# Optimization experiments

Hardware: AMD Instinct MI355X
Metric: run time of the kernel (lower is better)

The kernel has to match this reference:

```python
import jax, jax.numpy as jnp
import numpy as np

DIM = 1024
N_HEADS = 16
HEAD_DIM = 64
SEQ = 2048
BATCH = 2


def setup_inputs() -> dict:
    key = jax.random.key(0)
    ks = jax.random.split(key, 7)
    scale = 1.0 / np.sqrt(DIM)
    return {
        "q": jax.random.normal(ks[0], (BATCH, SEQ, DIM), dtype=jnp.float32),
        "k": jax.random.normal(ks[1], (BATCH, SEQ, DIM), dtype=jnp.float32),
        "v": jax.random.normal(ks[2], (BATCH, SEQ, DIM), dtype=jnp.float32),
        "wq": jax.random.normal(ks[3], (DIM, DIM), dtype=jnp.float32) * scale,
        "wk": jax.random.normal(ks[4], (DIM, DIM), dtype=jnp.float32) * scale,
        "wv": jax.random.normal(ks[5], (DIM, DIM), dtype=jnp.float32) * scale,
        "wo": jax.random.normal(ks[6], (DIM, DIM), dtype=jnp.float32) * scale,
    }


def reference(q, k, v, wq, wk, wv, wo):
    B, S, D = q.shape
    # Linear layers: y = x @ W.T (torch nn.Linear convention)
    qh = (q @ wq.T).reshape(B, S, N_HEADS, HEAD_DIM).transpose(0, 2, 1, 3)  # [B,H,S,hd]
    kh = (k @ wk.T).reshape(B, S, N_HEADS, HEAD_DIM).transpose(0, 2, 1, 3)
    vh = (v @ wv.T).reshape(B, S, N_HEADS, HEAD_DIM).transpose(0, 2, 1, 3)
    score = jnp.einsum('bhqd,bhkd->bhqk', qh, kh) / jnp.sqrt(jnp.float32(HEAD_DIM))
    # causal mask: upper triangle (j > i) set to -inf
    causal = jnp.tril(jnp.ones((S, S), dtype=bool))
    score = jnp.where(causal[None, None], score, -jnp.inf)
    attn = jax.nn.softmax(score, axis=-1)
    out = jnp.einsum('bhqk,bhkd->bhqd', attn, vh)  # [B,H,S,hd]
    out = out.transpose(0, 2, 1, 3).reshape(B, S, D)
    return out @ wo.T
```

## Files before the change

kernel.cpp:

```cpp
#include <hip/hip_runtime.h>

typedef unsigned short u16;
typedef unsigned int   u32;
typedef __bf16 bf16x8 __attribute__((ext_vector_type(8)));
typedef float  f32x4  __attribute__((ext_vector_type(4)));
typedef unsigned short u16x4 __attribute__((ext_vector_type(4)));
typedef unsigned short u16x8 __attribute__((ext_vector_type(8)));
typedef unsigned int   u32x2 __attribute__((ext_vector_type(2)));
typedef unsigned int   u32x4 __attribute__((ext_vector_type(4)));

#define DIM   1024
#define SEQ   2048
#define NH    16
#define HD    64
#define NBATCH 2

#define NEG_INF (-__builtin_inff())


__device__ __forceinline__ u16 f2bf(float f) {
  unsigned u = __float_as_uint(f);
  unsigned r = (u + 0x7FFFu + ((u >> 16) & 1u)) >> 16;
  return (u16)r;
}

__device__ __forceinline__ void gload16(const void* g, void* lds_uniform) {
  __builtin_amdgcn_global_load_lds(
      (__attribute__((address_space(1))) void*)(size_t)g,
      (__attribute__((address_space(3))) void*)lds_uniform,
      16, 0, 0);
}


__global__ __launch_bounds__(256) void cvt_all(
    const float* __restrict__ q, const float* __restrict__ k, const float* __restrict__ v,
    const float* __restrict__ wq, const float* __restrict__ wk, const float* __restrict__ wv,
    const float* __restrict__ wo, u16* __restrict__ ws) {
  const size_t M = 1u << 20;
  int b = blockIdx.x;
  const float* src;
  u16* dst;
  int idx;
  if (b < 6144) {
    int t = b >> 11; idx = b & 2047;
    src = (t == 0) ? q : (t == 1) ? k : v;
    dst = ws + (size_t)t * 4 * M;
  } else {
    int t = (b - 6144) >> 9; idx = (b - 6144) & 511;
    src = (t == 0) ? wq : (t == 1) ? wk : (t == 2) ? wv : wo;
    dst = ws + (12 + (size_t)t) * M;
  }
  size_t i = ((size_t)idx * 256 + threadIdx.x) * 8;
  float4 a = *(const float4*)(src + i);
  float4 c = *(const float4*)(src + i + 4);
  u16x8 o;
  o[0] = f2bf(a.x); o[1] = f2bf(a.y); o[2] = f2bf(a.z); o[3] = f2bf(a.w);
  o[4] = f2bf(c.x); o[5] = f2bf(c.y); o[6] = f2bf(c.z); o[7] = f2bf(c.w);
  *(u16x8*)(dst + i) = o;
}


__device__ __forceinline__ void gemm128_core(const u16* __restrict__ A,
                                             const u16* __restrict__ W,
                                             u16* lds, f32x4 (&acc)[4][4]) {
  const int K = 1024;
  const int tid = threadIdx.x;
  const int wave = tid >> 6, lane = tid & 63;
  const int quad = lane >> 4, l15 = lane & 15;
  const int warp_m = wave >> 1, warp_n = wave & 1;
  const int bm = blockIdx.y, bn = blockIdx.x;

  const int c0 = wave * 128 + lane, c1 = c0 + 64;
  const u16* Ag0 = A + (size_t)(bm * 128 + (c0 >> 2)) * K + (c0 & 3) * 8;
  const u16* Ag1 = A + (size_t)(bm * 128 + (c1 >> 2)) * K + (c1 & 3) * 8;
  const u16* Wg0 = W + (size_t)(bn * 128 + (c0 >> 2)) * K + (c0 & 3) * 8;
  const u16* Wg1 = W + (size_t)(bn * 128 + (c1 >> 2)) * K + (c1 & 3) * 8;
  u16* lA0 = lds + (wave * 2 + 0) * 512;
  u16* lA1 = lds + (wave * 2 + 1) * 512;
  u16* lB0 = lds + 4096 + (wave * 2 + 0) * 512;
  u16* lB1 = lds + 4096 + (wave * 2 + 1) * 512;

  for (int k0 = 0; k0 < K; k0 += 32) {
    gload16(Ag0 + k0, lA0);
    gload16(Ag1 + k0, lA1);
    gload16(Wg0 + k0, lB0);
    gload16(Wg1 + k0, lB1);
    __syncthreads();

    bf16x8 af[4], bfr[4];
#pragma unroll
    for (int i = 0; i < 4; ++i) {
      af[i]  = *(const bf16x8*)(lds + (warp_m * 64 + i * 16 + l15) * 32 + quad * 8);
      bfr[i] = *(const bf16x8*)(lds + 4096 + (warp_n * 64 + i * 16 + l15) * 32 + quad * 8);
    }
#pragma unroll
    for (int i = 0; i < 4; ++i)
#pragma unroll
      for (int j = 0; j < 4; ++j)
        acc[i][j] = __builtin_amdgcn_mfma_f32_16x16x32_bf16(af[i], bfr[j], acc[i][j], 0, 0, 0);
    __syncthreads();
  }
}

__global__ __launch_bounds__(256) void gemm_qkv(
    const u16* __restrict__ qb, const u16* __restrict__ kb, const u16* __restrict__ vb,
    const u16* __restrict__ wq, const u16* __restrict__ wk, const u16* __restrict__ wv,
    u16* __restrict__ Qo, u16* __restrict__ Ko, u16* __restrict__ Vt) {
  __shared__ __align__(16) u16 lds[8192];
  const int z = blockIdx.z;
  const u16* A = (z == 0) ? qb : (z == 1) ? kb : vb;
  const u16* W = (z == 0) ? wq : (z == 1) ? wk : wv;
  f32x4 acc[4][4] = {};
  gemm128_core(A, W, lds, acc);

  const int tid = threadIdx.x;
  const int wave = tid >> 6, lane = tid & 63;
  const int quad = lane >> 4, l15 = lane & 15;
  const int warp_m = wave >> 1, warp_n = wave & 1;
  const int bm = blockIdx.y, bn = blockIdx.x;
#pragma unroll
  for (int i = 0; i < 4; ++i)
#pragma unroll
    for (int j = 0; j < 4; ++j) {
      int s0 = bm * 128 + warp_m * 64 + i * 16 + quad * 4;
      int n  = bn * 128 + warp_n * 64 + j * 16 + l15;
      int bb = s0 >> 11, sl0 = s0 & 2047, h = n >> 6, d = n & 63;
      if (z == 2) {
        int ssw = (sl0 & ~63) | ((((sl0 >> 3) & 7) ^ (d & 7)) << 3) | (sl0 & 7);
        u16x4 pv;
        pv[0] = f2bf(acc[i][j][0]); pv[1] = f2bf(acc[i][j][1]);
        pv[2] = f2bf(acc[i][j][2]); pv[3] = f2bf(acc[i][j][3]);
        *(u16x4*)(Vt + ((size_t)(bb * NH + h) * HD + d) * SEQ + ssw) = pv;
      } else if (z == 1) {
#pragma unroll
        for (int r = 0; r < 4; ++r) {
          int s = sl0 + r;
          int dsw = (((d >> 3) ^ (s & 7)) << 3) | (d & 7);
          Ko[((size_t)(bb * NH + h) * SEQ + s) * HD + dsw] = f2bf(acc[i][j][r]);
        }
      } else {
#pragma unroll
        for (int r = 0; r < 4; ++r)
          Qo[((size_t)(bb * NH + h) * SEQ + sl0 + r) * HD + d] = f2bf(acc[i][j][r] * 0.125f);
      }
    }
}

__global__ __launch_bounds__(256) void gemm_out(
    const u16* __restrict__ A, const u16* __restrict__ W, float* __restrict__ Out) {
  __shared__ __align__(16) u16 lds[8192];
  f32x4 acc[4][4] = {};
  gemm128_core(A, W, lds, acc);

  const int tid = threadIdx.x;
  const int wave = tid >> 6, lane = tid & 63;
  const int quad = lane >> 4, l15 = lane & 15;
  const int warp_m = wave >> 1, warp_n = wave & 1;
  const int bm = blockIdx.y, bn = blockIdx.x;
#pragma unroll
  for (int i = 0; i < 4; ++i)
#pragma unroll
    for (int j = 0; j < 4; ++j)
#pragma unroll
      for (int r = 0; r < 4; ++r) {
        int m = bm * 128 + warp_m * 64 + i * 16 + quad * 4 + r;
        int n = bn * 128 + warp_n * 64 + j * 16 + l15;
        Out[(size_t)m * DIM + n] = acc[i][j][r];
      }
}


__global__ __launch_bounds__(256) void attn_kernel(
    const u16* __restrict__ Q, const u16* __restrict__ K,
    const u16* __restrict__ Vt, u16* __restrict__ O) {
  __shared__ __align__(16) u16 Kl[2][4096];
  __shared__ __align__(16) u16 Vl[2][4096];
  __shared__ __align__(16) u32 Plm[4][16 * 36];

  const int tid = threadIdx.x;
  const int wave = tid >> 6, lane = tid & 63;
  const int quad = lane >> 4, l15 = lane & 15;
  const int bx = blockIdx.x;
  const int bh = bx & 31;
  const int qt = 31 - (bx >> 5);
  const int b = bh >> 4, h = bh & 15;

  const u16* qbase = Q + ((size_t)bh * SEQ + qt * 64 + wave * 16 + l15) * HD + quad * 8;
  const bf16x8 qf0 = *(const bf16x8*)(qbase);
  const bf16x8 qf1 = *(const bf16x8*)(qbase + 32);

  f32x4 o[4] = {};
  float l_sum = 0.f, m_run = NEG_INF;

  const int c0 = wave * 128 + lane, c1 = c0 + 64;
  const u16* Ksrc = K + (size_t)bh * SEQ * HD;
  const u16* Vsrc = Vt + (size_t)bh * HD * SEQ;
  const int sw0 = ((quad ^ (l15 & 7)) << 3);
  const int sw1 = (((4 + quad) ^ (l15 & 7)) << 3);

  {
    gload16(Ksrc + (size_t)c0 * 8, &Kl[0][(wave * 2 + 0) * 512]);
    gload16(Ksrc + (size_t)c1 * 8, &Kl[0][(wave * 2 + 1) * 512]);
    gload16(Vsrc + (size_t)(c0 >> 3) * SEQ + (c0 & 7) * 8, &Vl[0][(wave * 2 + 0) * 512]);
    gload16(Vsrc + (size_t)(c1 >> 3) * SEQ + (c1 & 7) * 8, &Vl[0][(wave * 2 + 1) * 512]);
  }

  u32* prow = &Plm[wave][l15 * 36];

  for (int kt = 0; kt <= qt; ++kt) {
    const int buf = kt & 1;
    __syncthreads();
    if (kt < qt) {
      const int nb = buf ^ 1;
      const size_t kb = (size_t)(kt + 1) * 64;
      gload16(Ksrc + (kb * HD) + (size_t)c0 * 8, &Kl[nb][(wave * 2 + 0) * 512]);
      gload16(Ksrc + (kb * HD) + (size_t)c1 * 8, &Kl[nb][(wave * 2 + 1) * 512]);
      gload16(Vsrc + (size_t)(c0 >> 3) * SEQ + kb + (c0 & 7) * 8, &Vl[nb][(wave * 2 + 0) * 512]);
      gload16(Vsrc + (size_t)(c1 >> 3) * SEQ + kb + (c1 & 7) * 8, &Vl[nb][(wave * 2 + 1) * 512]);
    }

    f32x4 s[4];
#pragma unroll
    for (int kn = 0; kn < 4; ++kn) {
      const u16* arow = &Kl[buf][(kn * 16 + l15) * 64];
      bf16x8 kf0 = *(const bf16x8*)(arow + sw0);
      bf16x8 kf1 = *(const bf16x8*)(arow + sw1);
      f32x4 z = {};
      z = __builtin_amdgcn_mfma_f32_16x16x32_bf16(kf0, qf0, z, 0, 0, 0);
      z = __builtin_amdgcn_mfma_f32_16x16x32_bf16(kf1, qf1, z, 0, 0, 0);
      s[kn] = z;
    }

    if (kt == qt) {
      const int qloc = wave * 16 + l15;
#pragma unroll
      for (int kn = 0; kn < 4; ++kn)
#pragma unroll
        for (int r = 0; r < 4; ++r)
          if (kn * 16 + quad * 4 + r > qloc) s[kn][r] = NEG_INF;
    }

    float mr = NEG_INF;
#pragma unroll
    for (int kn = 0; kn < 4; ++kn)
#pragma unroll
      for (int r = 0; r < 4; ++r) mr = fmaxf(mr, s[kn][r]);
    mr = fmaxf(mr, __shfl_xor(mr, 16));
    mr = fmaxf(mr, __shfl_xor(mr, 32));
    const float mnew = fmaxf(m_run, mr);
    const float alpha = __expf(m_run - mnew);
    m_run = mnew;
    float rs = 0.f;
#pragma unroll
    for (int kn = 0; kn < 4; ++kn)
#pragma unroll
      for (int r = 0; r < 4; ++r) {
        float p = __expf(s[kn][r] - mnew);
        s[kn][r] = p;
        rs += p;
      }
    rs += __shfl_xor(rs, 16);
    rs += __shfl_xor(rs, 32);
    l_sum = l_sum * alpha + rs;

    float aT[4];
#pragma unroll
    for (int r = 0; r < 4; ++r) aT[r] = __shfl(alpha, quad * 4 + r);
#pragma unroll
    for (int n = 0; n < 4; ++n)
#pragma unroll
      for (int r = 0; r < 4; ++r) o[n][r] *= aT[r];

#pragma unroll
    for (int kn = 0; kn < 4; ++kn) {
      u32x2 w;
      w[0] = (u32)f2bf(s[kn][0]) | ((u32)f2bf(s[kn][1]) << 16);
      w[1] = (u32)f2bf(s[kn][2]) | ((u32)f2bf(s[kn][3]) << 16);
      *(u32x2*)(prow + kn * 8 + quad * 2) = w;
    }
    u32x4 t0 = *(const u32x4*)(prow + quad * 4);
    u32x4 t1 = *(const u32x4*)(prow + 16 + quad * 4);
    bf16x8 pf0 = __builtin_bit_cast(bf16x8, t0);
    bf16x8 pf1 = __builtin_bit_cast(bf16x8, t1);

#pragma unroll
    for (int n = 0; n < 4; ++n) {
      const u16* vrow = &Vl[buf][(n * 16 + l15) * 64];
      bf16x8 vf0 = *(const bf16x8*)(vrow + sw0);
      bf16x8 vf1 = *(const bf16x8*)(vrow + sw1);
      o[n] = __builtin_amdgcn_mfma_f32_16x16x32_bf16(pf0, vf0, o[n], 0, 0, 0);
      o[n] = __builtin_amdgcn_mfma_f32_16x16x32_bf16(pf1, vf1, o[n], 0, 0, 0);
    }
  }

  float inv = 1.f / l_sum;
  float iT[4];
#pragma unroll
  for (int r = 0; r < 4; ++r) iT[r] = __shfl(inv, quad * 4 + r);
#pragma unroll
  for (int r = 0; r < 4; ++r) {
    int srow = qt * 64 + wave * 16 + quad * 4 + r;
#pragma unroll
    for (int n = 0; n < 4; ++n) {
      int col = h * HD + n * 16 + l15;
      O[((size_t)b * SEQ + srow) * DIM + col] = f2bf(o[n][r] * iT[r]);
    }
  }
}


extern "C" void kernel_launch(void* const* d_in, const int* in_sizes, int n_in,
                              void* d_out, int out_size, void* d_ws, size_t ws_size,
                              hipStream_t stream) {
  (void)in_sizes; (void)n_in; (void)out_size; (void)ws_size;
  const float* q  = (const float*)d_in[0];
  const float* k  = (const float*)d_in[1];
  const float* v  = (const float*)d_in[2];
  const float* wq = (const float*)d_in[3];
  const float* wk = (const float*)d_in[4];
  const float* wv = (const float*)d_in[5];
  const float* wv2 = (const float*)d_in[5];
  const float* wo = (const float*)d_in[6];
  (void)wv2;

  u16* ws = (u16*)d_ws;
  const size_t EL = 1u << 20;
  u16* QB = ws + 0 * EL;
  u16* KB = ws + 4 * EL;
  u16* VB = ws + 8 * EL;
  u16* WQ = ws + 12 * EL;
  u16* WK = ws + 13 * EL;
  u16* WV = ws + 14 * EL;
  u16* WO = ws + 15 * EL;
  u16* Qw = ws + 16 * EL;
  u16* Kw = ws + 20 * EL;
  u16* Vtw = ws + 24 * EL;
  u16* AO = ws + 28 * EL;

  cvt_all<<<8192, 256, 0, stream>>>(q, k, v, wq, wk, wv, wo, ws);
  gemm_qkv<<<dim3(8, 32, 3), 256, 0, stream>>>(QB, KB, VB, WQ, WK, WV, Qw, Kw, Vtw);
  attn_kernel<<<1024, 256, 0, stream>>>(Qw, Kw, Vtw, AO);
  gemm_out<<<dim3(8, 32), 256, 0, stream>>>(AO, WO, (float*)d_out);
}
```

Before: 232.9 us.

## Double-buffer GEMM LDS tiles and remap block IDs for L2 locality

```diff
diff --git a/kernel.cpp b/kernel.cpp
--- a/kernel.cpp
+++ b/kernel.cpp
@@ -62,43 +62,52 @@
 
 __device__ __forceinline__ void gemm128_core(const u16* __restrict__ A,
                                              const u16* __restrict__ W,
+                                             int bm, int bn,
                                              u16* lds, f32x4 (&acc)[4][4]) {
   const int K = 1024;
   const int tid = threadIdx.x;
   const int wave = tid >> 6, lane = tid & 63;
   const int quad = lane >> 4, l15 = lane & 15;
   const int warp_m = wave >> 1, warp_n = wave & 1;
-  const int bm = blockIdx.y, bn = blockIdx.x;
 
   const int c0 = wave * 128 + lane, c1 = c0 + 64;
   const u16* Ag0 = A + (size_t)(bm * 128 + (c0 >> 2)) * K + (c0 & 3) * 8;
   const u16* Ag1 = A + (size_t)(bm * 128 + (c1 >> 2)) * K + (c1 & 3) * 8;
   const u16* Wg0 = W + (size_t)(bn * 128 + (c0 >> 2)) * K + (c0 & 3) * 8;
   const u16* Wg1 = W + (size_t)(bn * 128 + (c1 >> 2)) * K + (c1 & 3) * 8;
-  u16* lA0 = lds + (wave * 2 + 0) * 512;
-  u16* lA1 = lds + (wave * 2 + 1) * 512;
-  u16* lB0 = lds + 4096 + (wave * 2 + 0) * 512;
-  u16* lB1 = lds + 4096 + (wave * 2 + 1) * 512;
+  const int lA0 = (wave * 2 + 0) * 512;
+  const int lA1 = (wave * 2 + 1) * 512;
+  const int lB0 = 4096 + (wave * 2 + 0) * 512;
+  const int lB1 = 4096 + (wave * 2 + 1) * 512;
+
+  gload16(Ag0, lds + lA0);
+  gload16(Ag1, lds + lA1);
+  gload16(Wg0, lds + lB0);
+  gload16(Wg1, lds + lB1);
 
   for (int k0 = 0; k0 < K; k0 += 32) {
-    gload16(Ag0 + k0, lA0);
-    gload16(Ag1 + k0, lA1);
-    gload16(Wg0 + k0, lB0);
-    gload16(Wg1 + k0, lB1);
+    const int buf = (k0 >> 5) & 1;
+    u16* cur = lds + buf * 8192;
     __syncthreads();
+    if (k0 + 32 < K) {
+      u16* nxt = lds + (buf ^ 1) * 8192;
+      gload16(Ag0 + k0 + 32, nxt + lA0);
+      gload16(Ag1 + k0 + 32, nxt + lA1);
+      gload16(Wg0 + k0 + 32, nxt + lB0);
+      gload16(Wg1 + k0 + 32, nxt + lB1);
+    }
 
     bf16x8 af[4], bfr[4];
 #pragma unroll
     for (int i = 0; i < 4; ++i) {
-      af[i]  = *(const bf16x8*)(lds + (warp_m * 64 + i * 16 + l15) * 32 + quad * 8);
-      bfr[i] = *(const bf16x8*)(lds + 4096 + (warp_n * 64 + i * 16 + l15) * 32 + quad * 8);
+      af[i]  = *(const bf16x8*)(cur + (warp_m * 64 + i * 16 + l15) * 32 + quad * 8);
+      bfr[i] = *(const bf16x8*)(cur + 4096 + (warp_n * 64 + i * 16 + l15) * 32 + quad * 8);
     }
 #pragma unroll
     for (int i = 0; i < 4; ++i)
 #pragma unroll
       for (int j = 0; j < 4; ++j)
         acc[i][j] = __builtin_amdgcn_mfma_f32_16x16x32_bf16(af[i], bfr[j], acc[i][j], 0, 0, 0);
-    __syncthreads();
   }
 }
 
@@ -106,18 +115,21 @@
     const u16* __restrict__ qb, const u16* __restrict__ kb, const u16* __restrict__ vb,
     const u16* __restrict__ wq, const u16* __restrict__ wk, const u16* __restrict__ wv,
     u16* __restrict__ Qo, u16* __restrict__ Ko, u16* __restrict__ Vt) {
-  __shared__ __align__(16) u16 lds[8192];
-  const int z = blockIdx.z;
+  __shared__ __align__(16) u16 lds[2][8192];
+  const int id = blockIdx.x;
+  const int c = id & 7, bn = (id >> 3) & 7, t = id >> 6;
+  const int g = c + 8 * t;
+  const int bm = g & 31, z = g >> 5;
+
   const u16* A = (z == 0) ? qb : (z == 1) ? kb : vb;
   const u16* W = (z == 0) ? wq : (z == 1) ? wk : wv;
   f32x4 acc[4][4] = {};
-  gemm128_core(A, W, lds, acc);
+  gemm128_core(A, W, bm, bn, &lds[0][0], acc);
 
   const int tid = threadIdx.x;
   const int wave = tid >> 6, lane = tid & 63;
   const int quad = lane >> 4, l15 = lane & 15;
   const int warp_m = wave >> 1, warp_n = wave & 1;
-  const int bm = blockIdx.y, bn = blockIdx.x;
 #pragma unroll
   for (int i = 0; i < 4; ++i)
 #pragma unroll
@@ -148,15 +160,17 @@
 
 __global__ __launch_bounds__(256) void gemm_out(
     const u16* __restrict__ A, const u16* __restrict__ W, float* __restrict__ Out) {
-  __shared__ __align__(16) u16 lds[8192];
+  __shared__ __align__(16) u16 lds[2][8192];
+  const int id = blockIdx.x;
+  const int bn = (id >> 3) & 7;
+  const int bm = (id & 7) + 8 * (id >> 6);
   f32x4 acc[4][4] = {};
-  gemm128_core(A, W, lds, acc);
+  gemm128_core(A, W, bm, bn, &lds[0][0], acc);
 
   const int tid = threadIdx.x;
   const int wave = tid >> 6, lane = tid & 63;
   const int quad = lane >> 4, l15 = lane & 15;
   const int warp_m = wave >> 1, warp_n = wave & 1;
-  const int bm = blockIdx.y, bn = blockIdx.x;
 #pragma unroll
   for (int i = 0; i < 4; ++i)
 #pragma unroll
@@ -319,9 +333,7 @@
   const float* wq = (const float*)d_in[3];
   const float* wk = (const float*)d_in[4];
   const float* wv = (const float*)d_in[5];
-  const float* wv2 = (const float*)d_in[5];
   const float* wo = (const float*)d_in[6];
-  (void)wv2;
 
   u16* ws = (u16*)d_ws;
   const size_t EL = 1u << 20;
@@ -338,7 +350,7 @@
   u16* AO = ws + 28 * EL;
 
   cvt_all<<<8192, 256, 0, stream>>>(q, k, v, wq, wk, wv, wo, ws);
-  gemm_qkv<<<dim3(8, 32, 3), 256, 0, stream>>>(QB, KB, VB, WQ, WK, WV, Qw, Kw, Vtw);
+  gemm_qkv<<<768, 256, 0, stream>>>(QB, KB, VB, WQ, WK, WV, Qw, Kw, Vtw);
   attn_kernel<<<1024, 256, 0, stream>>>(Qw, Kw, Vtw, AO);
-  gemm_out<<<dim3(8, 32), 256, 0, stream>>>(AO, WO, (float*)d_out);
-}
+  gemm_out<<<256, 256, 0, stream>>>(AO, WO, (float*)d_out);
+}
```

After: 203.2 us. -12.8%, faster.
